# Kernel optimization log

Measured on AMD Instinct MI355X. Metric: run time of the kernel, lower is better.

The kernel has to match this reference:

```python
import jax, jax.numpy as jnp
import numpy as np

WINDOW_SIZE = 11
CHANNEL = 1
SIGMA = 1.5


def _gaussian_1d(size, sigma):
    coords = jnp.arange(size, dtype=jnp.float32) - size // 2
    g = jnp.exp(-coords ** 2 / (2 * sigma ** 2))
    return g / g.sum()


def _window_3d(size, channel, sigma=SIGMA):
    g = _gaussian_1d(size, sigma)
    w3 = g[:, None, None] * g[None, :, None] * g[None, None, :]  # [K,K,K]
    # OIDHW with groups=channel -> [channel, 1, K, K, K]
    return jnp.broadcast_to(w3[None, None], (channel, 1, size, size, size))


def _conv3d(x, window, channel):
    pad = WINDOW_SIZE // 2
    return jax.lax.conv_general_dilated(
        x, window,
        window_strides=(1, 1, 1),
        padding=[(pad, pad)] * 3,
        dimension_numbers=('NCDHW', 'OIDHW', 'NCDHW'),
        feature_group_count=channel,
    )


def setup_inputs() -> dict:
    key = jax.random.key(0)
    k1, k2 = jax.random.split(key)
    shape = (4, 1, 128, 128, 128)
    img1 = jax.random.uniform(k1, shape, dtype=jnp.float32)
    img2 = jax.random.uniform(k2, shape, dtype=jnp.float32)
    return {"img1": img1, "img2": img2}


def reference(img1, img2):
    channel = img1.shape[1]
    window = _window_3d(WINDOW_SIZE, channel).astype(img1.dtype)

    mu1 = _conv3d(img1, window, channel)
    mu2 = _conv3d(img2, window, channel)
    mu1_sq = mu1 * mu1
    mu2_sq = mu2 * mu2
    mu1_mu2 = mu1 * mu2

    sigma1_sq = _conv3d(img1 * img1, window, channel) - mu1_sq
    sigma2_sq = _conv3d(img2 * img2, window, channel) - mu2_sq
    sigma12 = _conv3d(img1 * img2, window, channel) - mu1_mu2

    C1 = 0.01 ** 2
    C2 = 0.03 ** 2
    ssim_map = ((2 * mu1_mu2 + C1) * (2 * sigma12 + C2)) / (
        (mu1_sq + mu2_sq + C1) * (sigma1_sq + sigma2_sq + C2))
    return ssim_map.mean()
```

## Files before the change

kernel.cpp:

```cpp
#include <hip/hip_runtime.h>
#include <hip/hip_fp16.h>
#include <math.h>

#define NB  4
#define DD  128
#define HH  128
#define WW  128
#define KS  11
#define PAD 5
#define NF  4
#define ZCK 32
#define HCK 32
#define RW  144
#define LOFF 6

#define QS      8
#define HROW    (64 * QS)
#define ZPLANE  (HH * HROW)

using f32x2 = __attribute__((ext_vector_type(2))) float;

struct GW { float g[KS]; };

static __device__ __forceinline__ f32x2 vfma2(f32x2 a, f32x2 b, f32x2 c) {
    return __builtin_elementwise_fma(a, b, c);
}
static __device__ __forceinline__ unsigned h2u(__half2 v) {
    union { __half2 h; unsigned u; } x; x.h = v; return x.u;
}
static __device__ __forceinline__ f32x2 u2f2(unsigned u) {
    union { unsigned u; __half2 h; } x; x.u = u;
    const float2 f = __half22float2(x.h);
    return (f32x2){f.x, f.y};
}

#define WAVE_LDS_FENCE() asm volatile("s_waitcnt lgkmcnt(0)" ::: "memory")

__global__ __launch_bounds__(256)
void k1_wd(const float* __restrict__ img1, const float* __restrict__ img2,
           __half* __restrict__ A, GW gw) {
    __shared__ alignas(16) float srow[2][2][4][RW];
    const int t  = threadIdx.x;
    const int b  = blockIdx.x;
    const int hb = b & 31;
    const int zc = (b >> 5) & 3;
    const int n  = b >> 7;
    const int r  = t >> 6;
    const int q  = t & 63;
    const int w0 = q * 2;
    const int h  = hb * 4 + r;
    const int z0 = zc * ZCK;

    if (q < 48) {
        const int grp = q / 12, s12 = q % 12;
        const int slot = (s12 < 6) ? s12 : (128 + s12);
        srow[grp >> 1][grp & 1][r][slot] = 0.f;
    }

    const long long inBase  = (long long)n * DD * HH * WW +
                              (long long)h * WW + w0;
    const long long outBase = (long long)n * DD * ZPLANE +
                              (long long)h * HROW + (long long)q * QS;

    f32x2 acc[NF][KS];
    #pragma unroll
    for (int f = 0; f < NF; ++f)
        #pragma unroll
        for (int j = 0; j < KS; ++j) acc[f][j] = (f32x2){0.f, 0.f};

    const int STEPS = ZCK + 2 * PAD;

    float2 rx0 = make_float2(0.f, 0.f), ry0 = rx0, rx1 = rx0, ry1 = rx0;
    {
        const int zi0 = z0 - PAD;
        if (zi0 >= 0) {
            const long long off = inBase + (long long)zi0 * (HH * WW);
            rx0 = *(const float2*)(img1 + off);
            ry0 = *(const float2*)(img2 + off);
        }
        const int zi1 = z0 - PAD + 1;
        if (zi1 >= 0) {
            const long long off = inBase + (long long)zi1 * (HH * WW);
            rx1 = *(const float2*)(img1 + off);
            ry1 = *(const float2*)(img2 + off);
        }
    }
    *(float2*)&srow[0][0][r][LOFF + w0] = rx0;
    *(float2*)&srow[0][1][r][LOFF + w0] = ry0;

    #define ELV(A2, i) ((i) & 1 ? A2[(i) >> 1].y : A2[(i) >> 1].x)

    #define K1_STEP(S, CUR, NXT, RXC, RYC, RXN, RYN, DOST)                     \
    {                                                                          \
              \
        WAVE_LDS_FENCE();                                                      \
        {           \
            const int zi = z0 - PAD + (S) + 2;                                 \
            float2 lx = make_float2(0.f, 0.f), ly = lx;                        \
            if ((S) + 2 < STEPS && zi >= 0 && zi < DD) {                       \
                const long long off = inBase + (long long)zi * (HH * WW);      \
                lx = *(const float2*)(img1 + off);                             \
                ly = *(const float2*)(img2 + off);                             \
            }                                                                  \
            RXC = lx; RYC = ly;                                                \
        }                                                                      \
             \
        f32x2 xv2[7], yv2[7];                                                  \
        _Pragma("unroll")                                                      \
        for (int i = 0; i < 7; ++i) {                                          \
            const float2 ax = *(const float2*)&srow[CUR][0][r][w0 + 2 * i];    \
            const float2 ay = *(const float2*)&srow[CUR][1][r][w0 + 2 * i];    \
            xv2[i] = (f32x2){ax.x, ax.y};                                      \
            yv2[i] = (f32x2){ay.x, ay.y};                                      \
        }                                                                      \
                                    \
        f32x2 pv2[7], qv2[7];                                                  \
        _Pragma("unroll")                                                      \
        for (int i = 0; i < 7; ++i) {                                          \
            pv2[i] = xv2[i] * yv2[i];                                          \
            qv2[i] = vfma2(yv2[i], yv2[i], xv2[i] * xv2[i]);                   \
        }                                                                      \
                            \
        float a0x = 0.f, a0y = 0.f, a1x = 0.f, a1y = 0.f;                      \
        float a2x = 0.f, a2y = 0.f, a3x = 0.f, a3y = 0.f;                      \
        _Pragma("unroll")                                                      \
        for (int k = 0; k < KS; ++k) {                                         \
            const float g = gw.g[k];                                           \
            a0x = fmaf(g, ELV(xv2, k + 1), a0x);                               \
            a0y = fmaf(g, ELV(xv2, k + 2), a0y);                               \
            a1x = fmaf(g, ELV(yv2, k + 1), a1x);                               \
            a1y = fmaf(g, ELV(yv2, k + 2), a1y);                               \
            a2x = fmaf(g, ELV(pv2, k + 1), a2x);                               \
            a2y = fmaf(g, ELV(pv2, k + 2), a2y);                               \
            a3x = fmaf(g, ELV(qv2, k + 1), a3x);                               \
            a3y = fmaf(g, ELV(qv2, k + 2), a3y);                               \
        }                                                                      \
              \
        *(float2*)&srow[NXT][0][r][LOFF + w0] = RXN;                           \
        *(float2*)&srow[NXT][1][r][LOFF + w0] = RYN;                           \
                                   \
        f32x2 v[NF];                                                           \
        v[0] = (f32x2){a0x, a0y}; v[1] = (f32x2){a1x, a1y};                    \
        v[2] = (f32x2){a2x, a2y}; v[3] = (f32x2){a3x, a3y};                    \
        _Pragma("unroll")                                                      \
        for (int f = 0; f < NF; ++f) {                                         \
            _Pragma("unroll")                                                  \
            for (int j = KS - 1; j >= 1; --j) {                                \
                const f32x2 gg = {gw.g[j], gw.g[j]};                           \
                acc[f][j] = vfma2(gg, v[f], acc[f][j - 1]);                    \
            }                                                                  \
            const f32x2 g0 = {gw.g[0], gw.g[0]};                               \
            acc[f][0] = g0 * v[f];                                             \
        }                                                                      \
        if (DOST) {                                                            \
            const int zo = z0 + (S) - 2 * PAD;                                 \
            uint4 pk;                                                          \
            pk.x = h2u(__float22half2_rn(                                      \
                       make_float2(acc[0][KS-1].x, acc[0][KS-1].y)));          \
            pk.y = h2u(__float22half2_rn(                                      \
                       make_float2(acc[1][KS-1].x, acc[1][KS-1].y)));          \
            pk.z = h2u(__float22half2_rn(                                      \
                       make_float2(acc[2][KS-1].x, acc[2][KS-1].y)));          \
            pk.w = h2u(__float22half2_rn(                                      \
                       make_float2(acc[3][KS-1].x, acc[3][KS-1].y)));          \
            *(uint4*)(A + outBase + (long long)zo * ZPLANE) = pk;              \
        }                                                                      \
    }

    for (int s2 = 0; s2 < 2 * PAD; s2 += 2) {
        K1_STEP(s2,     0, 1, rx0, ry0, rx1, ry1, 0)
        K1_STEP(s2 + 1, 1, 0, rx1, ry1, rx0, ry0, 0)
    }
    for (int s2 = 2 * PAD; s2 < STEPS; s2 += 2) {
        K1_STEP(s2,     0, 1, rx0, ry0, rx1, ry1, 1)
        K1_STEP(s2 + 1, 1, 0, rx1, ry1, rx0, ry0, 1)
    }
    #undef K1_STEP
    #undef ELV
}

__global__ __launch_bounds__(256)
void k2_hssim(const __half* __restrict__ A, double* __restrict__ partials,
              GW gw) {
    const int t  = threadIdx.x;
    const int b  = blockIdx.x;
    const int hc = b & 3;
    const int zp = (b >> 2) & 31;
    const int n  = b >> 7;
    const int zl = t >> 6;
    const int q  = t & 63;
    const int z  = zp * 4 + zl;
    const int h0 = hc * HCK;

    const long long colBase =
        ((long long)(n * DD + z)) * ZPLANE + (long long)q * QS;

    f32x2 acc[NF][KS];
    #pragma unroll
    for (int f = 0; f < NF; ++f)
        #pragma unroll
        for (int j = 0; j < KS; ++j) acc[f][j] = (f32x2){0.f, 0.f};

    const int STEPS = HCK + 2 * PAD;

    uint4 pfA = make_uint4(0u, 0u, 0u, 0u), pfB = pfA;
    {
        const int hi0 = h0 - PAD;
        if (hi0 >= 0)
            pfA = *(const uint4*)(A + colBase + (long long)hi0 * HROW);
        const int hi1 = h0 - PAD + 1;
        if (hi1 >= 0)
            pfB = *(const uint4*)(A + colBase + (long long)hi1 * HROW);
    }

    const f32x2 C1v = {1e-4f, 1e-4f}, C2v = {9e-4f, 9e-4f};
    const f32x2 TWO = {2.f, 2.f};
    f32x2 sum = {0.f, 0.f};

    #define K2_STEP(S, PFC, DOSSIM)                                            \
    {                                                                          \
        f32x2 v[NF];                                                           \
        v[0] = u2f2(PFC.x); v[1] = u2f2(PFC.y);                                \
        v[2] = u2f2(PFC.z); v[3] = u2f2(PFC.w);                                \
        {                                                \
            const int hi = h0 - PAD + (S) + 2;                                 \
            uint4 nv = make_uint4(0u, 0u, 0u, 0u);                             \
            if ((S) + 2 < STEPS && hi >= 0 && hi < HH)                         \
                nv = *(const uint4*)(A + colBase + (long long)hi * HROW);      \
            PFC = nv;                                                          \
        }                                                                      \
        _Pragma("unroll")                                                      \
        for (int f = 0; f < NF; ++f) {                                         \
            _Pragma("unroll")                                                  \
            for (int j = KS - 1; j >= 1; --j) {                                \
                const f32x2 gg = {gw.g[j], gw.g[j]};                           \
                acc[f][j] = vfma2(gg, v[f], acc[f][j - 1]);                    \
            }                                                                  \
            const f32x2 g0 = {gw.g[0], gw.g[0]};                               \
            acc[f][0] = g0 * v[f];                                             \
        }                                                                      \
        if (DOSSIM) {                                                          \
            const f32x2 mu1 = acc[0][KS - 1], mu2 = acc[1][KS - 1];            \
            const f32x2 mu1s = mu1 * mu1, mu2s = mu2 * mu2, mu12 = mu1 * mu2;  \
            const f32x2 sg12 = acc[2][KS - 1] - mu12;                          \
            const f32x2 sgss = acc[3][KS - 1] - mu1s - mu2s;                   \
            const f32x2 num = vfma2(TWO, mu12, C1v) * vfma2(TWO, sg12, C2v);   \
            const f32x2 den = (mu1s + mu2s + C1v) * (sgss + C2v);              \
            f32x2 rr;                                                          \
            rr.x = __builtin_amdgcn_rcpf(den.x);                               \
            rr.y = __builtin_amdgcn_rcpf(den.y);                               \
            rr = rr * vfma2(-den, rr, TWO);                     \
            sum = vfma2(num, rr, sum);                                         \
        }                                                                      \
    }

    for (int s2 = 0; s2 < 2 * PAD; s2 += 2) {
        K2_STEP(s2,     pfA, 0)
        K2_STEP(s2 + 1, pfB, 0)
    }
    for (int s2 = 2 * PAD; s2 < STEPS; s2 += 2) {
        K2_STEP(s2,     pfA, 1)
        K2_STEP(s2 + 1, pfB, 1)
    }
    #undef K2_STEP

    __shared__ double red[256];
    red[t] = (double)sum.x + (double)sum.y;
    __syncthreads();
    for (int sft = 128; sft > 0; sft >>= 1) {
        if (t < sft) red[t] += red[t + sft];
        __syncthreads();
    }
    if (t == 0) partials[b] = red[0];
}

__global__ __launch_bounds__(256)
void k4_reduce(const double* __restrict__ partials, int nPart,
               float* __restrict__ out) {
    __shared__ double red[256];
    const int t = threadIdx.x;
    double s = 0.0;
    for (int i = t; i < nPart; i += 256) s += partials[i];
    red[t] = s;
    __syncthreads();
    for (int sft = 128; sft > 0; sft >>= 1) {
        if (t < sft) red[t] += red[t + sft];
        __syncthreads();
    }
    if (t == 0) out[0] = (float)(red[0] / (double)((long long)NB * DD * HH * WW));
}

extern "C" void kernel_launch(void* const* d_in, const int* in_sizes, int n_in,
                              void* d_out, int out_size, void* d_ws, size_t ws_size,
                              hipStream_t stream) {
    const float* img1 = (const float*)d_in[0];
    const float* img2 = (const float*)d_in[1];
    float* out = (float*)d_out;

    GW gw;
    {
        double gs[KS], ssum = 0.0;
        for (int i = 0; i < KS; ++i) {
            const double c = (double)(i - KS / 2);
            gs[i] = exp(-c * c / (2.0 * 1.5 * 1.5));
            ssum += gs[i];
        }
        for (int i = 0; i < KS; ++i) gw.g[i] = (float)(gs[i] / ssum);
    }

    __half* A = (__half*)d_ws;
    double* partials =
        (double*)((char*)d_ws + (long long)NB * DD * ZPLANE * sizeof(__half));

    const int nBlocksK1 = NB * 32 * (DD / ZCK);
    const int nBlocksK2 = NB * 32 * (HH / HCK);

    k1_wd<<<nBlocksK1, 256, 0, stream>>>(img1, img2, A, gw);
    k2_hssim<<<nBlocksK2, 256, 0, stream>>>(A, partials, gw);
    k4_reduce<<<1, 256, 0, stream>>>(partials, nBlocksK2, out);
}
```

Measured before the change: 58.27 us.

## Halve z/h chunk sizes, interleave x/y in LDS, and combine squared channels

Halves the z-chunk and h-chunk per block so twice as many blocks launch, and raises launch bounds to request 4 blocks per SIMD. Interleaves img1/img2 in shared memory so one float4 load serves both images. The W-pass now filters x²+y² as one channel and x·y as another, using packed FMAs, and the output channels are repacked. Smaller chunks add more halo recompute per output (10 extra z planes per 16 instead of per 32), and the occupancy hint may force register spills.

```diff
diff --git a/kernel.cpp b/kernel.cpp
--- a/kernel.cpp
+++ b/kernel.cpp
@@ -9,10 +9,9 @@
 #define KS  11
 #define PAD 5
 #define NF  4
-#define ZCK 32
-#define HCK 32
-#define RW  144
-#define LOFF 6
+#define ZCK 16
+#define HCK 16
+#define RWI 140
 
 #define QS      8
 #define HROW    (64 * QS)
@@ -36,25 +35,26 @@
 
 #define WAVE_LDS_FENCE() asm volatile("s_waitcnt lgkmcnt(0)" ::: "memory")
 
-__global__ __launch_bounds__(256)
+__global__ __launch_bounds__(256, 4)
 void k1_wd(const float* __restrict__ img1, const float* __restrict__ img2,
            __half* __restrict__ A, GW gw) {
-    __shared__ alignas(16) float srow[2][2][4][RW];
+    __shared__ alignas(16) float srow[2][4][RWI][2];
     const int t  = threadIdx.x;
     const int b  = blockIdx.x;
     const int hb = b & 31;
-    const int zc = (b >> 5) & 3;
-    const int n  = b >> 7;
+    const int zc = (b >> 5) & 7;
+    const int n  = b >> 8;
     const int r  = t >> 6;
     const int q  = t & 63;
     const int w0 = q * 2;
     const int h  = hb * 4 + r;
     const int z0 = zc * ZCK;
 
-    if (q < 48) {
-        const int grp = q / 12, s12 = q % 12;
-        const int slot = (s12 < 6) ? s12 : (128 + s12);
-        srow[grp >> 1][grp & 1][r][slot] = 0.f;
+    if (q < 24) {
+        const int buf = q / 12, i12 = q % 12;
+        const int slot = (i12 < 6) ? i12 : (128 + i12);
+        srow[buf][r][slot][0] = 0.f;
+        srow[buf][r][slot][1] = 0.f;
     }
 
     const long long inBase  = (long long)n * DD * HH * WW +
@@ -62,11 +62,12 @@
     const long long outBase = (long long)n * DD * ZPLANE +
                               (long long)h * HROW + (long long)q * QS;
 
-    f32x2 acc[NF][KS];
+    f32x2 cA0[KS], cA1[KS], cB0[KS], cB1[KS];
     #pragma unroll
-    for (int f = 0; f < NF; ++f)
-        #pragma unroll
-        for (int j = 0; j < KS; ++j) acc[f][j] = (f32x2){0.f, 0.f};
+    for (int j = 0; j < KS; ++j) {
+        cA0[j] = (f32x2){0.f, 0.f}; cA1[j] = (f32x2){0.f, 0.f};
+        cB0[j] = (f32x2){0.f, 0.f}; cB1[j] = (f32x2){0.f, 0.f};
+    }
 
     const int STEPS = ZCK + 2 * PAD;
 
@@ -85,14 +86,22 @@
             ry1 = *(const float2*)(img2 + off);
         }
     }
-    *(float2*)&srow[0][0][r][LOFF + w0] = rx0;
-    *(float2*)&srow[0][1][r][LOFF + w0] = ry0;
-
-    #define ELV(A2, i) ((i) & 1 ? A2[(i) >> 1].y : A2[(i) >> 1].x)
+    {
+        float4 st; st.x = rx0.x; st.y = ry0.x; st.z = rx0.y; st.w = ry0.y;
+        *(float4*)&srow[0][r][w0 + 6][0] = st;
+    }
+
+    #define DCHAIN(ACC, V)                                                     \
+        _Pragma("unroll")                                                      \
+        for (int j = KS - 1; j >= 1; --j) {                                    \
+            const f32x2 gg = {gw.g[j], gw.g[j]};                               \
+            ACC[j] = vfma2(gg, V, ACC[j - 1]);                                 \
+        }                                                                      \
+        { const f32x2 g0 = {gw.g[0], gw.g[0]}; ACC[0] = g0 * (V); }
 
     #define K1_STEP(S, CUR, NXT, RXC, RYC, RXN, RYN, DOST)                     \
     {                                                                          \
-              \
+               \
         WAVE_LDS_FENCE();                                                      \
         {           \
             const int zi = z0 - PAD + (S) + 2;                                 \
@@ -105,64 +114,55 @@
             RXC = lx; RYC = ly;                                                \
         }                                                                      \
              \
-        f32x2 xv2[7], yv2[7];                                                  \
+        f32x2 pair_[14]; f32x2 qsq_[14]; float pxy_[14];                       \
         _Pragma("unroll")                                                      \
         for (int i = 0; i < 7; ++i) {                                          \
-            const float2 ax = *(const float2*)&srow[CUR][0][r][w0 + 2 * i];    \
-            const float2 ay = *(const float2*)&srow[CUR][1][r][w0 + 2 * i];    \
-            xv2[i] = (f32x2){ax.x, ax.y};                                      \
-            yv2[i] = (f32x2){ay.x, ay.y};                                      \
-        }                                                                      \
-                                    \
-        f32x2 pv2[7], qv2[7];                                                  \
-        _Pragma("unroll")                                                      \
-        for (int i = 0; i < 7; ++i) {                                          \
-            pv2[i] = xv2[i] * yv2[i];                                          \
-            qv2[i] = vfma2(yv2[i], yv2[i], xv2[i] * xv2[i]);                   \
-        }                                                                      \
-                            \
-        float a0x = 0.f, a0y = 0.f, a1x = 0.f, a1y = 0.f;                      \
-        float a2x = 0.f, a2y = 0.f, a3x = 0.f, a3y = 0.f;                      \
+            const float4 v = *(const float4*)&srow[CUR][r][w0 + 2 * i][0];     \
+            pair_[2*i]   = (f32x2){v.x, v.y};                                  \
+            pair_[2*i+1] = (f32x2){v.z, v.w};                                  \
+            qsq_[2*i]    = pair_[2*i] * pair_[2*i];                            \
+            qsq_[2*i+1]  = pair_[2*i+1] * pair_[2*i+1];                        \
+            pxy_[2*i]    = v.x * v.y;                                          \
+            pxy_[2*i+1]  = v.z * v.w;                                          \
+        }                                                                      \
+                                      \
+        f32x2 c01_0 = {0.f, 0.f}, c01_1 = {0.f, 0.f};                          \
+        f32x2 cQ_0  = {0.f, 0.f}, cQ_1  = {0.f, 0.f};                          \
+        float c2_0 = 0.f, c2_1 = 0.f;                                          \
         _Pragma("unroll")                                                      \
         for (int k = 0; k < KS; ++k) {                                         \
             const float g = gw.g[k];                                           \
-            a0x = fmaf(g, ELV(xv2, k + 1), a0x);                               \
-            a0y = fmaf(g, ELV(xv2, k + 2), a0y);                               \
-            a1x = fmaf(g, ELV(yv2, k + 1), a1x);                               \
-            a1y = fmaf(g, ELV(yv2, k + 2), a1y);                               \
-            a2x = fmaf(g, ELV(pv2, k + 1), a2x);                               \
-            a2y = fmaf(g, ELV(pv2, k + 2), a2y);                               \
-            a3x = fmaf(g, ELV(qv2, k + 1), a3x);                               \
-            a3y = fmaf(g, ELV(qv2, k + 2), a3y);                               \
+            const f32x2 gg = {g, g};                                           \
+            c01_0 = vfma2(gg, pair_[k + 1], c01_0);                            \
+            c01_1 = vfma2(gg, pair_[k + 2], c01_1);                            \
+            cQ_0  = vfma2(gg, qsq_[k + 1], cQ_0);                              \
+            cQ_1  = vfma2(gg, qsq_[k + 2], cQ_1);                              \
+            c2_0  = fmaf(g, pxy_[k + 1], c2_0);                                \
+            c2_1  = fmaf(g, pxy_[k + 2], c2_1);                                \
         }                                                                      \
               \
-        *(float2*)&srow[NXT][0][r][LOFF + w0] = RXN;                           \
-        *(float2*)&srow[NXT][1][r][LOFF + w0] = RYN;                           \
-                                   \
-        f32x2 v[NF];                                                           \
-        v[0] = (f32x2){a0x, a0y}; v[1] = (f32x2){a1x, a1y};                    \
-        v[2] = (f32x2){a2x, a2y}; v[3] = (f32x2){a3x, a3y};                    \
-        _Pragma("unroll")                                                      \
-        for (int f = 0; f < NF; ++f) {                                         \
-            _Pragma("unroll")                                                  \
-            for (int j = KS - 1; j >= 1; --j) {                                \
-                const f32x2 gg = {gw.g[j], gw.g[j]};                           \
-                acc[f][j] = vfma2(gg, v[f], acc[f][j - 1]);                    \
-            }                                                                  \
-            const f32x2 g0 = {gw.g[0], gw.g[0]};                               \
-            acc[f][0] = g0 * v[f];                                             \
-        }                                                                      \
+        {                                                                      \
+            float4 st; st.x = RXN.x; st.y = RYN.x; st.z = RXN.y; st.w = RYN.y; \
+            *(float4*)&srow[NXT][r][w0 + 6][0] = st;                           \
+        }                                                                      \
+                                                     \
+        const f32x2 vB0 = {c2_0, cQ_0.x + cQ_0.y};                             \
+        const f32x2 vB1 = {c2_1, cQ_1.x + cQ_1.y};                             \
+        DCHAIN(cA0, c01_0)                                                     \
+        DCHAIN(cA1, c01_1)                                                     \
+        DCHAIN(cB0, vB0)                                                       \
+        DCHAIN(cB1, vB1)                                                       \
         if (DOST) {                                                            \
             const int zo = z0 + (S) - 2 * PAD;                                 \
             uint4 pk;                                                          \
             pk.x = h2u(__float22half2_rn(                                      \
-                       make_float2(acc[0][KS-1].x, acc[0][KS-1].y)));          \
+                       make_float2(cA0[KS-1].x, cA1[KS-1].x)));     \
             pk.y = h2u(__float22half2_rn(                                      \
-                       make_float2(acc[1][KS-1].x, acc[1][KS-1].y)));          \
+                       make_float2(cA0[KS-1].y, cA1[KS-1].y)));     \
             pk.z = h2u(__float22half2_rn(                                      \
-                       make_float2(acc[2][KS-1].x, acc[2][KS-1].y)));          \
+                       make_float2(cB0[KS-1].x, cB1[KS-1].x)));     \
             pk.w = h2u(__float22half2_rn(                                      \
-                       make_float2(acc[3][KS-1].x, acc[3][KS-1].y)));          \
+                       make_float2(cB0[KS-1].y, cB1[KS-1].y)));     \
             *(uint4*)(A + outBase + (long long)zo * ZPLANE) = pk;              \
         }                                                                      \
     }
@@ -176,17 +176,17 @@
         K1_STEP(s2 + 1, 1, 0, rx1, ry1, rx0, ry0, 1)
     }
     #undef K1_STEP
-    #undef ELV
-}
-
-__global__ __launch_bounds__(256)
+    #undef DCHAIN
+}
+
+__global__ __launch_bounds__(256, 4)
 void k2_hssim(const __half* __restrict__ A, double* __restrict__ partials,
               GW gw) {
     const int t  = threadIdx.x;
     const int b  = blockIdx.x;
-    const int hc = b & 3;
-    const int zp = (b >> 2) & 31;
-    const int n  = b >> 7;
+    const int hc = b & 7;
+    const int zp = (b >> 3) & 31;
+    const int n  = b >> 8;
     const int zl = t >> 6;
     const int q  = t & 63;
     const int z  = zp * 4 + zl;
```

New measurement: 143.2 us. 2.46x slower.

## Use single-wave k1 blocks with four-slot LDS ring and deeper prefetch

Applied to the files above, without the earlier changes.

The first kernel now launches one 64-thread wave per block, one h row each, instead of 4 waves per block covering 4 rows. The LDS staging becomes a 4-slot ring: two z-planes are written per iteration and global loads are issued two planes ahead. This halves the number of LDS fences and gives loads more time to land, at the cost of more live prefetch registers and 4x more, smaller blocks.

```diff
diff --git a/kernel.cpp b/kernel.cpp
--- a/kernel.cpp
+++ b/kernel.cpp
@@ -36,25 +36,23 @@
 
 #define WAVE_LDS_FENCE() asm volatile("s_waitcnt lgkmcnt(0)" ::: "memory")
 
-__global__ __launch_bounds__(256)
+__global__ __launch_bounds__(64)
 void k1_wd(const float* __restrict__ img1, const float* __restrict__ img2,
            __half* __restrict__ A, GW gw) {
-    __shared__ alignas(16) float srow[2][2][4][RW];
-    const int t  = threadIdx.x;
+    __shared__ alignas(16) float srow[4][2][RW];
+    const int q  = threadIdx.x;
     const int b  = blockIdx.x;
-    const int hb = b & 31;
-    const int zc = (b >> 5) & 3;
-    const int n  = b >> 7;
-    const int r  = t >> 6;
-    const int q  = t & 63;
+    const int h  = b & 127;
+    const int zc = (b >> 7) & 3;
+    const int n  = b >> 9;
     const int w0 = q * 2;
-    const int h  = hb * 4 + r;
     const int z0 = zc * ZCK;
 
     if (q < 48) {
         const int grp = q / 12, s12 = q % 12;
         const int slot = (s12 < 6) ? s12 : (128 + s12);
-        srow[grp >> 1][grp & 1][r][slot] = 0.f;
+        srow[grp >> 1][grp & 1][slot] = 0.f;
+        srow[2 + (grp >> 1)][grp & 1][slot] = 0.f;
     }
 
     const long long inBase  = (long long)n * DD * HH * WW +
@@ -70,57 +68,60 @@
 
     const int STEPS = ZCK + 2 * PAD;
 
-    float2 rx0 = make_float2(0.f, 0.f), ry0 = rx0, rx1 = rx0, ry1 = rx0;
+    const float2 FZ = make_float2(0.f, 0.f);
+    float2 sx0 = FZ, sy0 = FZ, sx1 = FZ, sy1 = FZ;
     {
         const int zi0 = z0 - PAD;
         if (zi0 >= 0) {
             const long long off = inBase + (long long)zi0 * (HH * WW);
-            rx0 = *(const float2*)(img1 + off);
-            ry0 = *(const float2*)(img2 + off);
+            sx0 = *(const float2*)(img1 + off);
+            sy0 = *(const float2*)(img2 + off);
         }
         const int zi1 = z0 - PAD + 1;
         if (zi1 >= 0) {
             const long long off = inBase + (long long)zi1 * (HH * WW);
-            rx1 = *(const float2*)(img1 + off);
-            ry1 = *(const float2*)(img2 + off);
-        }
-    }
-    *(float2*)&srow[0][0][r][LOFF + w0] = rx0;
-    *(float2*)&srow[0][1][r][LOFF + w0] = ry0;
+            sx1 = *(const float2*)(img1 + off);
+            sy1 = *(const float2*)(img2 + off);
+        }
+    }
+    *(float2*)&srow[0][0][LOFF + w0] = sx0;
+    *(float2*)&srow[0][1][LOFF + w0] = sy0;
+    *(float2*)&srow[1][0][LOFF + w0] = sx1;
+    *(float2*)&srow[1][1][LOFF + w0] = sy1;
+    float2 p2x = FZ, p2y = FZ, p3x = FZ, p3y = FZ;
+    {
+        const int zi2 = z0 - PAD + 2;
+        if (zi2 >= 0 && zi2 < DD) {
+            const long long off = inBase + (long long)zi2 * (HH * WW);
+            p2x = *(const float2*)(img1 + off);
+            p2y = *(const float2*)(img2 + off);
+        }
+        const int zi3 = z0 - PAD + 3;
+        if (zi3 >= 0 && zi3 < DD) {
+            const long long off = inBase + (long long)zi3 * (HH * WW);
+            p3x = *(const float2*)(img1 + off);
+            p3y = *(const float2*)(img2 + off);
+        }
+    }
 
     #define ELV(A2, i) ((i) & 1 ? A2[(i) >> 1].y : A2[(i) >> 1].x)
 
-    #define K1_STEP(S, CUR, NXT, RXC, RYC, RXN, RYN, DOST)                     \
+    #define STEPBODY(S, BUF, DOST)                                             \
     {                                                                          \
-              \
-        WAVE_LDS_FENCE();                                                      \
-        {           \
-            const int zi = z0 - PAD + (S) + 2;                                 \
-            float2 lx = make_float2(0.f, 0.f), ly = lx;                        \
-            if ((S) + 2 < STEPS && zi >= 0 && zi < DD) {                       \
-                const long long off = inBase + (long long)zi * (HH * WW);      \
-                lx = *(const float2*)(img1 + off);                             \
-                ly = *(const float2*)(img2 + off);                             \
-            }                                                                  \
-            RXC = lx; RYC = ly;                                                \
-        }                                                                      \
-             \
         f32x2 xv2[7], yv2[7];                                                  \
         _Pragma("unroll")                                                      \
         for (int i = 0; i < 7; ++i) {                                          \
-            const float2 ax = *(const float2*)&srow[CUR][0][r][w0 + 2 * i];    \
-            const float2 ay = *(const float2*)&srow[CUR][1][r][w0 + 2 * i];    \
+            const float2 ax = *(const float2*)&srow[BUF][0][w0 + 2 * i];       \
+            const float2 ay = *(const float2*)&srow[BUF][1][w0 + 2 * i];       \
             xv2[i] = (f32x2){ax.x, ax.y};                                      \
             yv2[i] = (f32x2){ay.x, ay.y};                                      \
         }                                                                      \
-                                    \
         f32x2 pv2[7], qv2[7];                                                  \
         _Pragma("unroll")                                                      \
         for (int i = 0; i < 7; ++i) {                                          \
             pv2[i] = xv2[i] * yv2[i];                                          \
             qv2[i] = vfma2(yv2[i], yv2[i], xv2[i] * xv2[i]);                   \
         }                                                                      \
-                            \
         float a0x = 0.f, a0y = 0.f, a1x = 0.f, a1y = 0.f;                      \
         float a2x = 0.f, a2y = 0.f, a3x = 0.f, a3y = 0.f;                      \
         _Pragma("unroll")                                                      \
@@ -135,10 +136,6 @@
             a3x = fmaf(g, ELV(qv2, k + 1), a3x);                               \
             a3y = fmaf(g, ELV(qv2, k + 2), a3y);                               \
         }                                                                      \
-              \
-        *(float2*)&srow[NXT][0][r][LOFF + w0] = RXN;                           \
-        *(float2*)&srow[NXT][1][r][LOFF + w0] = RYN;                           \
-                                   \
         f32x2 v[NF];                                                           \
         v[0] = (f32x2){a0x, a0y}; v[1] = (f32x2){a1x, a1y};                    \
         v[2] = (f32x2){a2x, a2y}; v[3] = (f32x2){a3x, a3y};                    \
@@ -167,15 +164,48 @@
         }                                                                      \
     }
 
-    for (int s2 = 0; s2 < 2 * PAD; s2 += 2) {
-        K1_STEP(s2,     0, 1, rx0, ry0, rx1, ry1, 0)
-        K1_STEP(s2 + 1, 1, 0, rx1, ry1, rx0, ry0, 0)
-    }
-    for (int s2 = 2 * PAD; s2 < STEPS; s2 += 2) {
-        K1_STEP(s2,     0, 1, rx0, ry0, rx1, ry1, 1)
-        K1_STEP(s2 + 1, 1, 0, rx1, ry1, rx0, ry0, 1)
-    }
-    #undef K1_STEP
+    #define K1_ITER(S, RA, RB, WA, WB, DOST)                                   \
+    {                                                                          \
+        WAVE_LDS_FENCE();           \
+        *(float2*)&srow[WA][0][LOFF + w0] = p2x;                               \
+        *(float2*)&srow[WA][1][LOFF + w0] = p2y;                               \
+        *(float2*)&srow[WB][0][LOFF + w0] = p3x;                               \
+        *(float2*)&srow[WB][1][LOFF + w0] = p3y;                               \
+        {        \
+            const int zi4 = z0 - PAD + (S) + 4;                                \
+            float2 lx = FZ, ly = FZ;                                           \
+            if ((S) + 4 < STEPS && zi4 >= 0 && zi4 < DD) {                     \
+                const long long off = inBase + (long long)zi4 * (HH * WW);     \
+                lx = *(const float2*)(img1 + off);                             \
+                ly = *(const float2*)(img2 + off);                             \
+            }                                                                  \
+            p2x = lx; p2y = ly;                                                \
+        }                                                                      \
+        {                                                                      \
+            const int zi5 = z0 - PAD + (S) + 5;                                \
+            float2 lx = FZ, ly = FZ;                                           \
+            if ((S) + 5 < STEPS && zi5 >= 0 && zi5 < DD) {                     \
+                const long long off = inBase + (long long)zi5 * (HH * WW);     \
+                lx = *(const float2*)(img1 + off);                             \
+                ly = *(const float2*)(img2 + off);                             \
+            }                                                                  \
+            p3x = lx; p3y = ly;                                                \
+        }                                                                      \
+        STEPBODY((S),     RA, DOST)                                            \
+        STEPBODY((S) + 1, RB, DOST)                                            \
+    }
+
+    K1_ITER(0, 0, 1, 2, 3, 0)
+    K1_ITER(2, 2, 3, 0, 1, 0)
+    K1_ITER(4, 0, 1, 2, 3, 0)
+    K1_ITER(6, 2, 3, 0, 1, 0)
+    K1_ITER(8, 0, 1, 2, 3, 0)
+    for (int s = 10; s < STEPS; s += 4) {
+        K1_ITER(s,     2, 3, 0, 1, 1)
+        K1_ITER(s + 2, 0, 1, 2, 3, 1)
+    }
+    #undef K1_ITER
+    #undef STEPBODY
     #undef ELV
 }
 
@@ -312,10 +342,10 @@
     double* partials =
         (double*)((char*)d_ws + (long long)NB * DD * ZPLANE * sizeof(__half));
 
-    const int nBlocksK1 = NB * 32 * (DD / ZCK);
+    const int nBlocksK1 = NB * HH * (DD / ZCK);
     const int nBlocksK2 = NB * 32 * (HH / HCK);
 
-    k1_wd<<<nBlocksK1, 256, 0, stream>>>(img1, img2, A, gw);
+    k1_wd<<<nBlocksK1, 64, 0, stream>>>(img1, img2, A, gw);
     k2_hssim<<<nBlocksK2, 256, 0, stream>>>(A, partials, gw);
     k4_reduce<<<1, 256, 0, stream>>>(partials, nBlocksK2, out);
 }
```

Measured after the change: 60.26 us. +3.4%, slower.

## Replace LDS row staging with buffer loads of overlapping windows in k1

Applied to the files above, without the earlier changes.

The first kernel no longer stages each input row in shared memory with a software double-buffer and prefetch. Each lane now loads its 7 overlapping float2 neighbours straight from global memory with raw buffer loads, using the buffer range check (record size set to 0 for out-of-range z) to get zero padding. Blocks shrink to one wave of 64 threads, with four times as many blocks. This drops LDS traffic and fences, but it issues seven times as many global loads per step and waits on vmcnt(0) every step, so the cross-step prefetch overlap is lost.

```diff
diff --git a/kernel.cpp b/kernel.cpp
--- a/kernel.cpp
+++ b/kernel.cpp
@@ -11,14 +11,13 @@
 #define NF  4
 #define ZCK 32
 #define HCK 32
-#define RW  144
-#define LOFF 6
 
 #define QS      8
 #define HROW    (64 * QS)
 #define ZPLANE  (HH * HROW)
 
 using f32x2 = __attribute__((ext_vector_type(2))) float;
+using u32x4 = __attribute__((ext_vector_type(4))) unsigned;
 
 struct GW { float g[KS]; };
 
@@ -34,33 +33,40 @@
     return (f32x2){f.x, f.y};
 }
 
-#define WAVE_LDS_FENCE() asm volatile("s_waitcnt lgkmcnt(0)" ::: "memory")
-
-__global__ __launch_bounds__(256)
+static __device__ __forceinline__ u32x4 make_rsrc(const float* p, unsigned bytes) {
+    const unsigned long long a = (unsigned long long)p;
+    u32x4 r;
+    r.x = __builtin_amdgcn_readfirstlane((unsigned)a);
+    r.y = __builtin_amdgcn_readfirstlane((unsigned)(a >> 32));
+    r.z = bytes;
+    r.w = 0x00020000u;
+    return r;
+}
+static __device__ __forceinline__ float2 bload2(u32x4 rsrc, unsigned voff) {
+    float2 r;
+    asm volatile("buffer_load_dwordx2 %0, %1, %2, 0 offen"
+                 : "=v"(r) : "v"(voff), "s"(rsrc));
+    return r;
+}
+
+__global__ __launch_bounds__(64)
 void k1_wd(const float* __restrict__ img1, const float* __restrict__ img2,
            __half* __restrict__ A, GW gw) {
-    __shared__ alignas(16) float srow[2][2][4][RW];
-    const int t  = threadIdx.x;
+    const int q  = threadIdx.x;
     const int b  = blockIdx.x;
-    const int hb = b & 31;
-    const int zc = (b >> 5) & 3;
-    const int n  = b >> 7;
-    const int r  = t >> 6;
-    const int q  = t & 63;
+    const int h  = b & 127;
+    const int zc = (b >> 7) & 3;
+    const int n  = b >> 9;
     const int w0 = q * 2;
-    const int h  = hb * 4 + r;
     const int z0 = zc * ZCK;
 
-    if (q < 48) {
-        const int grp = q / 12, s12 = q % 12;
-        const int slot = (s12 < 6) ? s12 : (128 + s12);
-        srow[grp >> 1][grp & 1][r][slot] = 0.f;
-    }
-
-    const long long inBase  = (long long)n * DD * HH * WW +
-                              (long long)h * WW + w0;
+    const long long nhBase  = (long long)n * DD * HH * WW + (long long)h * WW;
     const long long outBase = (long long)n * DD * ZPLANE +
                               (long long)h * HROW + (long long)q * QS;
+
+    unsigned vo[7];
+    #pragma unroll
+    for (int i = 0; i < 7; ++i) vo[i] = (unsigned)((w0 - 6 + 2 * i) * 4);
 
     f32x2 acc[NF][KS];
     #pragma unroll
@@ -70,53 +76,28 @@
 
     const int STEPS = ZCK + 2 * PAD;
 
-    float2 rx0 = make_float2(0.f, 0.f), ry0 = rx0, rx1 = rx0, ry1 = rx0;
-    {
-        const int zi0 = z0 - PAD;
-        if (zi0 >= 0) {
-            const long long off = inBase + (long long)zi0 * (HH * WW);
-            rx0 = *(const float2*)(img1 + off);
-            ry0 = *(const float2*)(img2 + off);
-        }
-        const int zi1 = z0 - PAD + 1;
-        if (zi1 >= 0) {
-            const long long off = inBase + (long long)zi1 * (HH * WW);
-            rx1 = *(const float2*)(img1 + off);
-            ry1 = *(const float2*)(img2 + off);
-        }
-    }
-    *(float2*)&srow[0][0][r][LOFF + w0] = rx0;
-    *(float2*)&srow[0][1][r][LOFF + w0] = ry0;
-
     #define ELV(A2, i) ((i) & 1 ? A2[(i) >> 1].y : A2[(i) >> 1].x)
 
-    #define K1_STEP(S, CUR, NXT, RXC, RYC, RXN, RYN, DOST)                     \
+    #define K1_STEP(S, DOST)                                                   \
     {                                                                          \
-              \
-        WAVE_LDS_FENCE();                                                      \
-        {           \
-            const int zi = z0 - PAD + (S) + 2;                                 \
-            float2 lx = make_float2(0.f, 0.f), ly = lx;                        \
-            if ((S) + 2 < STEPS && zi >= 0 && zi < DD) {                       \
-                const long long off = inBase + (long long)zi * (HH * WW);      \
-                lx = *(const float2*)(img1 + off);                             \
-                ly = *(const float2*)(img2 + off);                             \
-            }                                                                  \
-            RXC = lx; RYC = ly;                                                \
-        }                                                                      \
-             \
-        f32x2 xv2[7], yv2[7];                                                  \
+        const int zi = z0 - PAD + (S);                                         \
+        const unsigned rec = (zi >= 0 && zi < DD) ? (WW * 4u) : 0u;            \
+        const float* row1 = img1 + nhBase + (long long)zi * (HH * WW);         \
+        const float* row2 = img2 + nhBase + (long long)zi * (HH * WW);         \
+        const u32x4 d1 = make_rsrc(row1, rec);                                 \
+        const u32x4 d2 = make_rsrc(row2, rec);                                 \
+        float2 xw[7], yw[7];                                                   \
+        _Pragma("unroll")                                                      \
+        for (int i = 0; i < 7; ++i) xw[i] = bload2(d1, vo[i]);                 \
+        _Pragma("unroll")                                                      \
+        for (int i = 0; i < 7; ++i) yw[i] = bload2(d2, vo[i]);                 \
+        asm volatile("s_waitcnt vmcnt(0)" ::: "memory");                       \
+        __builtin_amdgcn_sched_barrier(0);                                     \
+        f32x2 xv2[7], yv2[7], pv2[7], qv2[7];                                  \
         _Pragma("unroll")                                                      \
         for (int i = 0; i < 7; ++i) {                                          \
-            const float2 ax = *(const float2*)&srow[CUR][0][r][w0 + 2 * i];    \
-            const float2 ay = *(const float2*)&srow[CUR][1][r][w0 + 2 * i];    \
-            xv2[i] = (f32x2){ax.x, ax.y};                                      \
-            yv2[i] = (f32x2){ay.x, ay.y};                                      \
-        }                                                                      \
-                                    \
-        f32x2 pv2[7], qv2[7];                                                  \
-        _Pragma("unroll")                                                      \
-        for (int i = 0; i < 7; ++i) {                                          \
+            xv2[i] = (f32x2){xw[i].x, xw[i].y};                                \
+            yv2[i] = (f32x2){yw[i].x, yw[i].y};                                \
             pv2[i] = xv2[i] * yv2[i];                                          \
             qv2[i] = vfma2(yv2[i], yv2[i], xv2[i] * xv2[i]);                   \
         }                                                                      \
@@ -135,9 +116,6 @@
             a3x = fmaf(g, ELV(qv2, k + 1), a3x);                               \
             a3y = fmaf(g, ELV(qv2, k + 2), a3y);                               \
         }                                                                      \
-              \
-        *(float2*)&srow[NXT][0][r][LOFF + w0] = RXN;                           \
-        *(float2*)&srow[NXT][1][r][LOFF + w0] = RYN;                           \
                                    \
         f32x2 v[NF];                                                           \
         v[0] = (f32x2){a0x, a0y}; v[1] = (f32x2){a1x, a1y};                    \
@@ -167,13 +145,11 @@
         }                                                                      \
     }
 
-    for (int s2 = 0; s2 < 2 * PAD; s2 += 2) {
-        K1_STEP(s2,     0, 1, rx0, ry0, rx1, ry1, 0)
-        K1_STEP(s2 + 1, 1, 0, rx1, ry1, rx0, ry0, 0)
-    }
-    for (int s2 = 2 * PAD; s2 < STEPS; s2 += 2) {
-        K1_STEP(s2,     0, 1, rx0, ry0, rx1, ry1, 1)
-        K1_STEP(s2 + 1, 1, 0, rx1, ry1, rx0, ry0, 1)
+    for (int s = 0; s < 2 * PAD; ++s) {
+        K1_STEP(s, 0)
+    }
+    for (int s = 2 * PAD; s < STEPS; ++s) {
+        K1_STEP(s, 1)
     }
     #undef K1_STEP
     #undef ELV
@@ -312,10 +288,10 @@
     double* partials =
         (double*)((char*)d_ws + (long long)NB * DD * ZPLANE * sizeof(__half));
 
-    const int nBlocksK1 = NB * 32 * (DD / ZCK);
+    const int nBlocksK1 = NB * HH * (DD / ZCK);
     const int nBlocksK2 = NB * 32 * (HH / HCK);
 
-    k1_wd<<<nBlocksK1, 256, 0, stream>>>(img1, img2, A, gw);
+    k1_wd<<<nBlocksK1, 64, 0, stream>>>(img1, img2, A, gw);
     k2_hssim<<<nBlocksK2, 256, 0, stream>>>(A, partials, gw);
     k4_reduce<<<1, 256, 0, stream>>>(partials, nBlocksK2, out);
 }
```

Result: slower. 63.54 us (+9.0%).
